# Kernel optimization log

Hardware: AMD Instinct MI355X
Metric: run time of the kernel (lower is better)

The kernel has to match this reference:

```python
import jax, jax.numpy as jnp
import numpy as np

B, T, K, H, KS = 8, 2048, 64, 8, 5
PAD = KS - 1  # causal left padding (kernel_size - stride, stride=1)


def setup_inputs() -> dict:
    key = jax.random.key(0)
    ks = jax.random.split(key, 6)
    s = 0.02
    return {
        "x": jax.random.normal(ks[0], (B, T, K), jnp.float32),
        "wq": jax.random.normal(ks[1], (K * H, K, KS), jnp.float32) * s,
        "bq": jnp.zeros((K * H,), jnp.float32),
        "wk": jax.random.normal(ks[2], (K * H, K, KS), jnp.float32) * s,
        "bk": jnp.zeros((K * H,), jnp.float32),
        "wv": jax.random.normal(ks[3], (K * H, K, KS), jnp.float32) * s,
        "wu": jax.random.normal(ks[4], (K, K * H), jnp.float32) * s,
        "bu": jnp.zeros((K,), jnp.float32),
    }


def _causal_conv(x_bkt, w, b=None):
    # x_bkt: [b, k, t]; w: [out_ch, in_ch, ks]; left-pad for causality
    y = jax.lax.conv_general_dilated(
        x_bkt, w, window_strides=(1,), padding=[(PAD, 0)],
        dimension_numbers=("NCH", "OIH", "NCH"))
    if b is not None:
        y = y + b[None, :, None]
    return y


def reference(x, wq, bq, wk, bk, wv, wu, bu):
    b, t, k = x.shape
    xc = jnp.transpose(x, (0, 2, 1))  # [b, k, t]
    # conv output channels k*h are viewed as (k, h): head index varies fastest
    q = _causal_conv(xc, wq, bq).reshape(b, k, H, t)
    kk = _causal_conv(xc, wk, bk).reshape(b, k, H, t)
    v = _causal_conv(xc, wv).reshape(b, k, H, t)
    scale = k ** 0.25
    # scores: [b, h, t_q, t_k]
    w = jnp.einsum("bdht,bdhs->bhts", q / scale, kk / scale)
    mask = jnp.triu(jnp.ones((t, t), bool), 1)  # mask_next=True, mask_diag=False
    w = jnp.where(mask[None, None], -jnp.inf, w)
    w = jax.nn.softmax(w, axis=-1)
    out = jnp.einsum("bhts,bdhs->bthd", w, v)  # [b, t, h, k]
    out = out.reshape(b, t, H * k)  # concat order (h outer, k inner)
    return out @ wu.T + bu
```

## Files before the change

### kernel.cpp

```cpp
#include <hip/hip_runtime.h>
#include <hip/hip_bf16.h>

typedef __attribute__((ext_vector_type(8))) short bf16x8;
typedef __attribute__((ext_vector_type(4))) float f32x4;
typedef __attribute__((ext_vector_type(16))) float f32x16;
typedef __attribute__((ext_vector_type(4))) unsigned int u32x4;
typedef __attribute__((ext_vector_type(2))) unsigned int u32x2;

#define Bn 8
#define Tn 2048
#define Kn 64
#define Hn 8
#define KSn 5
#define CHn 512
#define TPADn 2052

__device__ __forceinline__ unsigned short f2bf(float f) {
    unsigned int x = __builtin_bit_cast(unsigned int, f);
    unsigned int r = (x + 0x7fffu + ((x >> 16) & 1u)) >> 16;
    return (unsigned short)r;
}

__device__ __forceinline__ unsigned int cvt_pk_bf16(float lo, float hi) {
    unsigned int r;
    asm("v_cvt_pk_bf16_f32 %0, %1, %2" : "=v"(r) : "v"(lo), "v"(hi));
    return r;
}

__device__ __forceinline__ float fast_exp2(float x) {
#if __has_builtin(__builtin_amdgcn_exp2f)
    return __builtin_amdgcn_exp2f(x);
#else
    float r;
    asm("v_exp_f32 %0, %1" : "=v"(r) : "v"(x));
    return r;
#endif
}

__device__ __forceinline__ float xhalf_max(float v) {
    return fmaxf(v, __shfl_xor(v, 32));
}
__device__ __forceinline__ float xhalf_add(float v) {
    return v + __shfl_xor(v, 32);
}

__device__ __forceinline__ u32x2 pl32swap(unsigned int x, unsigned int y) {
#if __has_builtin(__builtin_amdgcn_permlane32_swap)
    return __builtin_amdgcn_permlane32_swap(x, y, false, false);
#else
    unsigned int xs = (unsigned int)__shfl_xor((int)x, 32);
    unsigned int ys = (unsigned int)__shfl_xor((int)y, 32);
    int hi = (threadIdx.x & 63) >> 5;
    u32x2 r;
    r[0] = hi ? ys : x;
    r[1] = hi ? y : xs;
    return r;
#endif
}

__device__ __forceinline__ void gload_lds16(const void* g, void* l) {
    __builtin_amdgcn_global_load_lds(
        (const __attribute__((address_space(1))) void*)g,
        (__attribute__((address_space(3))) void*)l, 16, 0, 0);
}

__global__ void prep_kernel(const float* __restrict__ x,
                            const float* __restrict__ wq, const float* __restrict__ bq,
                            const float* __restrict__ wk, const float* __restrict__ bk,
                            const float* __restrict__ wv,
                            const float* __restrict__ wu,
                            unsigned short* __restrict__ x_pad,
                            unsigned short* __restrict__ w2q, unsigned short* __restrict__ w2k,
                            unsigned short* __restrict__ w2v,
                            unsigned short* __restrict__ wu_b,
                            float* __restrict__ bqs, float* __restrict__ bks)
{
    const float inv_scale = 0.424660900144f;
    const int N0 = Bn*TPADn*Kn;
    const int N1 = KSn*CHn*Kn;
    const int total = N0 + 3*N1 + CHn*Kn + 2*CHn;
    for (int i = blockIdx.x*blockDim.x + threadIdx.x; i < total; i += gridDim.x*blockDim.x) {
        if (i < N0) {
            int b = i / (TPADn*Kn);
            int rem = i - b*(TPADn*Kn);
            int p = rem >> 6, ic = rem & 63;
            x_pad[i] = (p < 4) ? (unsigned short)0
                               : f2bf(x[((size_t)b*Tn + (p - 4))*Kn + ic]);
            continue;
        }
        int r = i - N0;
        if (r < 3*N1) {
            int conv = r / N1; int rr = r - conv*N1;
            int j = rr / (CHn*Kn); int rc = rr - j*(CHn*Kn);
            int c = rc >> 6; int ic = rc & 63;
            const float* w = (conv==0) ? wq : ((conv==1) ? wk : wv);
            float s = (conv==2) ? 1.0f : inv_scale;
            unsigned short* dst = (conv==0) ? w2q : ((conv==1) ? w2k : w2v);
            dst[rr] = f2bf(w[(c*Kn + ic)*KSn + j] * s);
            continue;
        }
        r -= 3*N1;
        if (r < CHn*Kn) { wu_b[r] = f2bf(wu[r]); continue; }
        r -= CHn*Kn;
        if (r < CHn) { bqs[r] = bq[r]*inv_scale; continue; }
        r -= CHn;
        bks[r] = bk[r]*inv_scale;
    }
}

__global__ __launch_bounds__(256) void conv_v4(
    const unsigned short* __restrict__ x_pad,
    const unsigned short* __restrict__ w2q, const unsigned short* __restrict__ w2k,
    const unsigned short* __restrict__ w2v,
    const float* __restrict__ bqs, const float* __restrict__ bks,
    unsigned short* __restrict__ q_s, unsigned short* __restrict__ k_s,
    unsigned short* __restrict__ v_t)
{
    __shared__ __align__(16) unsigned short xs[2][72*64];
    __shared__ __align__(16) unsigned short ts[64*64];
    const int tg = blockIdx.x;
    const int c0 = blockIdx.y * 64;
    const int zz = blockIdx.z;
    const int conv = zz >> 3, b = zz & 7;
    const unsigned short* w2 = (conv==0) ? w2q : ((conv==1) ? w2k : w2v);
    const float* bias = (conv==0) ? bqs : ((conv==1) ? bks : nullptr);
    unsigned short* outp = (conv==0) ? q_s : ((conv==1) ? k_s : v_t);
    const int tid = threadIdx.x;
    const int wid = tid >> 6, l = tid & 63;
    const int lr = l & 15, lh = l >> 4;
    const int wt = wid & 1, wc = wid >> 1;

    bf16x8 wf[5][2][2];
    #pragma unroll
    for (int j = 0; j < 5; ++j)
        #pragma unroll
        for (int kk = 0; kk < 2; ++kk)
            #pragma unroll
            for (int n2 = 0; n2 < 2; ++n2)
                wf[j][kk][n2] = *(const bf16x8*)
                    &w2[(j*CHn + c0 + wc*32 + n2*16 + lr)*Kn + kk*32 + lh*8];
    float bv0 = bias ? bias[c0 + wc*32 + lr]      : 0.0f;
    float bv1 = bias ? bias[c0 + wc*32 + 16 + lr] : 0.0f;

    const int swz_row = l >> 3;
    const int src_inrow = ((l & 7) << 4) ^ (swz_row << 4);

    int buf = 0;
    {
        const char* base = (const char*)(x_pad + (size_t)b*TPADn*Kn);
        int p0 = tg*256;
        for (int i = wid; i < 9; i += 4) {
            const char* src = base + (size_t)(p0 + i*8 + swz_row)*128 + src_inrow;
            gload_lds16(src, (char*)&xs[0][0] + i*1024);
        }
    }
    __syncthreads();

    for (int tt = 0; tt < 4; ++tt) {
        const int t0 = (tg*4 + tt)*64;
        if (tt < 3) {
            const char* base = (const char*)(x_pad + (size_t)b*TPADn*Kn);
            int p0 = t0 + 64;
            for (int i = wid; i < 9; i += 4) {
                const char* src = base + (size_t)(p0 + i*8 + swz_row)*128 + src_inrow;
                gload_lds16(src, (char*)&xs[buf^1][0] + i*1024);
            }
        }
        const char* xb = (const char*)&xs[buf][0];
        f32x4 acc[2][2] = {};
        #pragma unroll
        for (int j = 0; j < 5; ++j)
            #pragma unroll
            for (int kk = 0; kk < 2; ++kk) {
                #pragma unroll
                for (int m = 0; m < 2; ++m) {
                    int row = wt*32 + m*16 + lr + j;
                    bf16x8 a = *(const bf16x8*)
                        (xb + row*128 + ((kk*64 + lh*16) ^ ((row & 7) << 4)));
                    acc[m][0] = __builtin_amdgcn_mfma_f32_16x16x32_bf16(a, wf[j][kk][0], acc[m][0], 0, 0, 0);
                    acc[m][1] = __builtin_amdgcn_mfma_f32_16x16x32_bf16(a, wf[j][kk][1], acc[m][1], 0, 0, 0);
                }
            }
        __syncthreads();
        #pragma unroll
        for (int m = 0; m < 2; ++m)
            #pragma unroll
            for (int n2 = 0; n2 < 2; ++n2) {
                float bv = n2 ? bv1 : bv0;
                int cl = wc*32 + n2*16 + lr;
                #pragma unroll
                for (int reg = 0; reg < 4; ++reg) {
                    int tl = wt*32 + m*16 + lh*4 + reg;
                    ts[(tl*64 + cl) ^ ((tl & 7) << 3)] = f2bf(acc[m][n2][reg] + bv);
                }
            }
        __syncthreads();
        if (conv < 2) {
            #pragma unroll
            for (int it = 0; it < 2; ++it) {
                int idx = tid + it*256;
                int tl = idx >> 3, hl = idx & 7;
                unsigned short tmp[8];
                #pragma unroll
                for (int dl = 0; dl < 8; ++dl)
                    tmp[dl] = ts[(tl*64 + hl + 8*dl) ^ ((tl & 7) << 3)];
                size_t el = ((size_t)(b*Hn + hl)*Tn + t0 + tl)*Kn + (c0 >> 3);
                *(u32x4*)&outp[el] = *(u32x4*)tmp;
            }
        } else {
            #pragma unroll
            for (int it = 0; it < 2; ++it) {
                int idx = tid + it*256;
                int tc = idx >> 6, cl2 = idx & 63;
                int hl = cl2 & 7, dl = cl2 >> 3;
                unsigned short tmp[8];
                #pragma unroll
                for (int i2 = 0; i2 < 8; ++i2)
                    tmp[i2] = ts[((tc*8 + i2)*64 + cl2) ^ (((tc*8 + i2) & 7) << 3)];
                size_t el = ((size_t)(b*Hn + hl)*Kn + (c0 >> 3) + dl)*Tn + t0 + tc*8;
                *(u32x4*)&outp[el] = *(u32x4*)tmp;
            }
        }
        buf ^= 1;
    }
}

__global__ __launch_bounds__(256, 4) void attn_kernel(
    const unsigned short* __restrict__ q_s, const unsigned short* __restrict__ k_s,
    const unsigned short* __restrict__ v_t, unsigned short* __restrict__ attn2)
{
    __shared__ __align__(16) unsigned char lds_raw[16384];
    const int tid = threadIdx.x;
    const int wid = tid >> 6, l = tid & 63;
    const int lq = l & 31, hi = l >> 5;
    const int bx = blockIdx.x;
    const int bh = (bx & 7)*8 + ((bx >> 3) & 7);
    const int s4g = (bx >> 6) & 3, g = bx >> 8;
    const int j = (g == 0) ? 15 - s4g : (g == 1) ? s4g : (g == 2) ? 8 + s4g : 7 - s4g;
    const int cmax = 4*j + 3;
    const int cw = 4*j + wid;
    const int qw = cw * 32;
    const unsigned short* qp = q_s + (size_t)bh*Tn*Kn;
    const char* kpc = (const char*)(k_s + (size_t)bh*Tn*Kn);
    const char* vpc = (const char*)(v_t + (size_t)bh*Kn*Tn);
    unsigned short* op = attn2 + (size_t)bh*Tn*Kn;
    const int qg = qw + lq;

    const int krow = wid*8 + (l >> 3);
    const char* kSrc0 = kpc + krow*128 + (((l & 7) ^ (krow & 7)) << 4);
    const char* vSrc0 = vpc + (size_t)krow*8192 + ((l >> 2) & 1)*4096
                      + ((((l & 3) ^ (krow & 3))) << 4);
    const int dstOff = wid*1024;
    auto stage = [&](int pp, int t) {
        gload_lds16(kSrc0 + (size_t)t*4096, lds_raw + pp*4096 + dstOff);
        gload_lds16(vSrc0 + (size_t)t*64,   lds_raw + 8192 + pp*4096 + dstOff);
    };

    bf16x8 qf[4];
    #pragma unroll
    for (int m = 0; m < 4; ++m)
        qf[m] = *(const bf16x8*)&qp[(qw + lq)*Kn + m*16 + hi*8];

    f32x16 o0 = (f32x16)(0.0f), o1 = (f32x16)(0.0f);
    float m_run = -1e30f, l_run = 0.f;

    const int kReadBase = lq*128;
    const int kReadSwz  = (lq & 7) << 4;
    const int vReadBase = (lq >> 1)*128 + (lq & 1)*64;
    const int vSwz = (lq >> 1) & 3;

    stage(0, 0);
    __syncthreads();
    int p = 0;
    for (int t = 0; t <= cmax; ++t) {
        if (t < cmax) stage(p ^ 1, t + 1);
        if (t <= cw) {
            const char* sK = (const char*)lds_raw + p*4096;
            const char* sV = (const char*)lds_raw + 8192 + p*4096;
            bf16x8 kbf[4], vbf[2][2];
            #pragma unroll
            for (int m = 0; m < 4; ++m)
                kbf[m] = *(const bf16x8*)(sK + kReadBase + ((m*32 + hi*16) ^ kReadSwz));
            #pragma unroll
            for (int dn = 0; dn < 2; ++dn)
                #pragma unroll
                for (int ks = 0; ks < 2; ++ks)
                    vbf[dn][ks] = *(const bf16x8*)
                        (sV + dn*2048 + vReadBase + (((ks*2 + hi) ^ vSwz) << 4));
            const int s0 = t*32;
            f32x16 s = (f32x16)(0.0f);
            __builtin_amdgcn_s_setprio(1);
            #pragma unroll
            for (int m = 0; m < 4; ++m)
                s = __builtin_amdgcn_mfma_f32_32x32x16_bf16(kbf[m], qf[m], s, 0, 0, 0);
            __builtin_amdgcn_s_setprio(0);
            if (t == cw) {
                #pragma unroll
                for (int r = 0; r < 16; ++r) {
                    int sg = s0 + (r & 3) + 8*(r >> 2) + 4*hi;
                    if (sg > qg) s[r] = -1e30f;
                }
            }
            float a8[8];
            #pragma unroll
            for (int r = 0; r < 8; ++r) a8[r] = fmaxf(s[r], s[r + 8]);
            float a4_0 = fmaxf(a8[0], a8[4]), a4_1 = fmaxf(a8[1], a8[5]);
            float a4_2 = fmaxf(a8[2], a8[6]), a4_3 = fmaxf(a8[3], a8[7]);
            float mt = fmaxf(fmaxf(a4_0, a4_1), fmaxf(a4_2, a4_3));
            mt = xhalf_max(mt);
            if (!__all(mt <= m_run + 8.0f)) {
                float mn = fmaxf(m_run, mt);
                float alpha = fast_exp2(m_run - mn);
                m_run = mn;
                l_run *= alpha;
                #pragma unroll
                for (int r = 0; r < 16; ++r) { o0[r] *= alpha; o1[r] *= alpha; }
            }
            float ps[4] = {0.f, 0.f, 0.f, 0.f};
            #pragma unroll
            for (int r = 0; r < 16; ++r) {
                float pv = fast_exp2(s[r] - m_run);
                s[r] = pv;
                ps[r & 3] += pv;
            }
            l_run += (ps[0] + ps[1]) + (ps[2] + ps[3]);
            unsigned int W[8];
            #pragma unroll
            for (int rp = 0; rp < 8; ++rp)
                W[rp] = cvt_pk_bf16(s[2*rp], s[2*rp + 1]);
            u32x4 bw[2];
            #pragma unroll
            for (int m = 0; m < 2; ++m)
                #pragma unroll
                for (int jp = 0; jp < 2; ++jp) {
                    u32x2 sw = pl32swap(W[jp + 4*m], W[jp + 4*m + 2]);
                    bw[m][jp]     = sw[0];
                    bw[m][jp + 2] = sw[1];
                }
            __builtin_amdgcn_s_setprio(1);
            o0 = __builtin_amdgcn_mfma_f32_32x32x16_bf16(vbf[0][0], __builtin_bit_cast(bf16x8, bw[0]), o0, 0, 0, 0);
            o0 = __builtin_amdgcn_mfma_f32_32x32x16_bf16(vbf[0][1], __builtin_bit_cast(bf16x8, bw[1]), o0, 0, 0, 0);
            o1 = __builtin_amdgcn_mfma_f32_32x32x16_bf16(vbf[1][0], __builtin_bit_cast(bf16x8, bw[0]), o1, 0, 0, 0);
            o1 = __builtin_amdgcn_mfma_f32_32x32x16_bf16(vbf[1][1], __builtin_bit_cast(bf16x8, bw[1]), o1, 0, 0, 0);
            __builtin_amdgcn_s_setprio(0);
        }
        __syncthreads();
        p ^= 1;
    }

    float l_full = xhalf_add(l_run);
    char* myLds = (char*)lds_raw + wid*4096;
    float inv_l = 1.0f / l_full;
    #pragma unroll
    for (int e = 0; e < 16; e += 2) {
        int dd = (e & 3) + 8*(e >> 2) + 4*hi;
        unsigned int wv0 = cvt_pk_bf16(o0[e]*inv_l, o0[e+1]*inv_l);
        *(unsigned int*)(myLds + ((lq*128 + dd*2)      ^ ((lq & 7) << 4))) = wv0;
        unsigned int wv1 = cvt_pk_bf16(o1[e]*inv_l, o1[e+1]*inv_l);
        *(unsigned int*)(myLds + ((lq*128 + 64 + dd*2) ^ ((lq & 7) << 4))) = wv1;
    }
    int q2 = l >> 1, hf = l & 1;
    #pragma unroll
    for (int o4 = 0; o4 < 4; ++o4) {
        u32x4 vr2 = *(u32x4*)(myLds + ((q2*128 + hf*64 + o4*16) ^ ((q2 & 7) << 4)));
        *(u32x4*)&op[(qw + q2)*Kn + hf*32 + o4*8] = vr2;
    }
}

__global__ __launch_bounds__(256) void proj_kernel(
    const unsigned short* __restrict__ attn, const unsigned short* __restrict__ wu_b,
    const float* __restrict__ bu, float* __restrict__ outp)
{
    __shared__ float red[4*16*66];
    const int r0 = blockIdx.x * 16;
    const int tid = threadIdx.x;
    const int w = tid >> 6, l = tid & 63;
    const int lr = l & 15, lh = l >> 4;
    f32x4 acc[4] = {};
    const int r = r0 + lr;
    const int bb = r >> 11, tt = r & 2047;
    #pragma unroll
    for (int ki = 0; ki < 4; ++ki) {
        int kk = w*4 + ki;
        int ch = kk*32 + lh*8;
        int hh = ch >> 6, dd = ch & 63;
        bf16x8 a = *(const bf16x8*)&attn[(size_t)((bb*Hn + hh)*Tn + tt)*Kn + dd];
        #pragma unroll
        for (int n = 0; n < 4; ++n) {
            bf16x8 bf = *(const bf16x8*)&wu_b[(n*16 + lr)*CHn + ch];
            acc[n] = __builtin_amdgcn_mfma_f32_16x16x32_bf16(a, bf, acc[n], 0, 0, 0);
        }
    }
    #pragma unroll
    for (int n = 0; n < 4; ++n)
        #pragma unroll
        for (int reg = 0; reg < 4; ++reg)
            red[w*1056 + (lh*4 + reg)*66 + n*16 + lr] = acc[n][reg];
    __syncthreads();
    #pragma unroll
    for (int it = 0; it < 4; ++it) {
        int idx = tid + it*256;
        int rl = idx >> 6, ko = idx & 63;
        float s = red[rl*66 + ko] + red[1056 + rl*66 + ko]
                + red[2112 + rl*66 + ko] + red[3168 + rl*66 + ko] + bu[ko];
        outp[(size_t)(r0 + rl)*Kn + ko] = s;
    }
}

extern "C" void kernel_launch(void* const* d_in, const int* in_sizes, int n_in,
                              void* d_out, int out_size, void* d_ws, size_t ws_size,
                              hipStream_t stream)
{
    const float* x  = (const float*)d_in[0];
    const float* wq = (const float*)d_in[1];
    const float* bq = (const float*)d_in[2];
    const float* wk = (const float*)d_in[3];
    const float* bk = (const float*)d_in[4];
    const float* wv = (const float*)d_in[5];
    const float* wu = (const float*)d_in[6];
    const float* bu = (const float*)d_in[7];
    float* outp = (float*)d_out;

    char* ws = (char*)d_ws;
    size_t off = 0;
    auto alloc = [&](size_t bytes) {
        char* p = ws + off;
        off = (off + bytes + 255) & ~(size_t)255;
        return p;
    };
    unsigned short* x_pad = (unsigned short*)alloc((size_t)Bn*TPADn*Kn*2);
    unsigned short* w2q  = (unsigned short*)alloc((size_t)KSn*CHn*Kn*2);
    unsigned short* w2k  = (unsigned short*)alloc((size_t)KSn*CHn*Kn*2);
    unsigned short* w2v  = (unsigned short*)alloc((size_t)KSn*CHn*Kn*2);
    unsigned short* wu_b = (unsigned short*)alloc((size_t)CHn*Kn*2);
    float*  bqs = (float*)alloc(CHn*4);
    float*  bks = (float*)alloc(CHn*4);
    unsigned short* q_s  = (unsigned short*)alloc((size_t)Bn*Hn*Tn*Kn*2);
    unsigned short* k_s  = (unsigned short*)alloc((size_t)Bn*Hn*Tn*Kn*2);
    unsigned short* v_t  = (unsigned short*)alloc((size_t)Bn*Hn*Tn*Kn*2);
    unsigned short* attn = (unsigned short*)alloc((size_t)Bn*Tn*CHn*2);

    prep_kernel<<<2048, 256, 0, stream>>>(x, wq, bq, wk, bk, wv, wu,
                                          x_pad, w2q, w2k, w2v, wu_b, bqs, bks);
    conv_v4<<<dim3(8, 8, 24), 256, 0, stream>>>(
        x_pad, w2q, w2k, w2v, bqs, bks, q_s, k_s, v_t);
    attn_kernel<<<1024, 256, 0, stream>>>(q_s, k_s, v_t, attn);
    proj_kernel<<<(Bn*Tn)/16, 256, 0, stream>>>(attn, wu_b, bu, outp);
}
```

Baseline: 113.7 us.

## Split long causal attention query blocks across KV halves with a merge kernel

Query blocks in the second half of the sequence now have their KV range split into two segments, each handled by its own workgroup. Each workgroup writes an unnormalized bf16 partial output plus its running max and sum to a scratch buffer, and a new merge kernel combines the two with a log-sum-exp rescale. The aim is to balance per-block work so the grid is no longer limited by the longest causal blocks. The cost is an extra kernel launch, scratch-buffer traffic, and bf16 rounding of the partial outputs before they are merged.

```diff
diff --git a/kernel.cpp b/kernel.cpp
--- a/kernel.cpp
+++ b/kernel.cpp
@@ -14,6 +14,7 @@
 #define KSn 5
 #define CHn 512
 #define TPADn 2052
+#define PSZ 4608
 
 __device__ __forceinline__ unsigned short f2bf(float f) {
     unsigned int x = __builtin_bit_cast(unsigned int, f);
@@ -227,18 +228,22 @@
 
 __global__ __launch_bounds__(256, 4) void attn_kernel(
     const unsigned short* __restrict__ q_s, const unsigned short* __restrict__ k_s,
-    const unsigned short* __restrict__ v_t, unsigned short* __restrict__ attn2)
+    const unsigned short* __restrict__ v_t, unsigned short* __restrict__ attn2,
+    char* __restrict__ pbuf)
 {
     __shared__ __align__(16) unsigned char lds_raw[16384];
     const int tid = threadIdx.x;
     const int wid = tid >> 6, l = tid & 63;
     const int lq = l & 31, hi = l >> 5;
     const int bx = blockIdx.x;
-    const int bh = (bx & 7)*8 + ((bx >> 3) & 7);
-    const int s4g = (bx >> 6) & 3, g = bx >> 8;
-    const int j = (g == 0) ? 15 - s4g : (g == 1) ? s4g : (g == 2) ? 8 + s4g : 7 - s4g;
-    const int cmax = 4*j + 3;
-    const int cw = 4*j + wid;
+    const int mm = bx >> 3;
+    const int bh = (bx & 7)*8 + (mm & 7);
+    const int kb = mm >> 3;
+    int q, t0, t1, seg, part;
+    if (kb < 8)       { q = 15 - kb; seg = 0; t0 = 0;  t1 = 32;      part = 1; }
+    else if (kb < 16) { q = 23 - kb; seg = 1; t0 = 32; t1 = 4*q + 4; part = 1; }
+    else              { q = 23 - kb; seg = 0; t0 = 0;  t1 = 4*q + 4; part = 0; }
+    const int cw = 4*q + wid;
     const int qw = cw * 32;
     const unsigned short* qp = q_s + (size_t)bh*Tn*Kn;
     const char* kpc = (const char*)(k_s + (size_t)bh*Tn*Kn);
@@ -269,11 +274,11 @@
     const int vReadBase = (lq >> 1)*128 + (lq & 1)*64;
     const int vSwz = (lq >> 1) & 3;
 
-    stage(0, 0);
+    stage(0, t0);
     __syncthreads();
     int p = 0;
-    for (int t = 0; t <= cmax; ++t) {
-        if (t < cmax) stage(p ^ 1, t + 1);
+    for (int t = t0; t < t1; ++t) {
+        if (t + 1 < t1) stage(p ^ 1, t + 1);
         if (t <= cw) {
             const char* sK = (const char*)lds_raw + p*4096;
             const char* sV = (const char*)lds_raw + 8192 + p*4096;
@@ -348,6 +353,22 @@
         p ^= 1;
     }
 
+    if (part) {
+        const int pidx = ((seg*64 + bh)*8 + (q - 8))*4 + wid;
+        char* pb = pbuf + (size_t)pidx*PSZ;
+        unsigned int* po32 = (unsigned int*)pb;
+        float* pml = (float*)(pb + 4096);
+        #pragma unroll
+        for (int e = 0; e < 16; e += 2) {
+            int dd = (e & 3) + 8*(e >> 2) + 4*hi;
+            po32[(dd >> 1)*32 + lq]        = cvt_pk_bf16(o0[e], o0[e+1]);
+            po32[((dd + 32) >> 1)*32 + lq] = cvt_pk_bf16(o1[e], o1[e+1]);
+        }
+        pml[l] = m_run;
+        pml[64 + l] = l_run;
+        return;
+    }
+
     float l_full = xhalf_add(l_run);
     char* myLds = (char*)lds_raw + wid*4096;
     float inv_l = 1.0f / l_full;
@@ -365,6 +386,52 @@
         u32x4 vr2 = *(u32x4*)(myLds + ((q2*128 + hf*64 + o4*16) ^ ((q2 & 7) << 4)));
         *(u32x4*)&op[(qw + q2)*Kn + hf*32 + o4*8] = vr2;
     }
+}
+
+__global__ __launch_bounds__(256) void merge_kernel(
+    const char* __restrict__ pbuf, unsigned short* __restrict__ attn2)
+{
+    const int bx = blockIdx.x;
+    const int bh = (bx & 7)*8 + ((bx >> 3) & 7);
+    const int qq = (bx >> 6) & 7;
+    const int tid = threadIdx.x;
+    const int wid = tid >> 6, l = tid & 63;
+    const int c = 4*(8 + qq) + wid;
+    const int qw = c*32;
+    const int lq2 = l >> 1, hd = l & 1;
+
+    const int p0i = ((0*64 + bh)*8 + qq)*4 + wid;
+    const int p1i = ((1*64 + bh)*8 + qq)*4 + wid;
+    const char* pb0 = pbuf + (size_t)p0i*PSZ;
+    const char* pb1 = pbuf + (size_t)p1i*PSZ;
+    const unsigned int* po0 = (const unsigned int*)pb0;
+    const unsigned int* po1 = (const unsigned int*)pb1;
+    const float* pml0 = (const float*)(pb0 + 4096);
+    const float* pml1 = (const float*)(pb1 + 4096);
+
+    float m0 = pml0[lq2], l0 = pml0[64 + lq2] + pml0[96 + lq2];
+    float m1 = pml1[lq2], l1 = pml1[64 + lq2] + pml1[96 + lq2];
+    float mf = fmaxf(m0, m1);
+    float w0 = fast_exp2(m0 - mf), w1 = fast_exp2(m1 - mf);
+    float inv_l = 1.0f / (w0*l0 + w1*l1);
+    w0 *= inv_l; w1 *= inv_l;
+
+    unsigned int outw[16];
+    #pragma unroll
+    for (int dpl = 0; dpl < 16; ++dpl) {
+        int dp = hd*16 + dpl;
+        unsigned int v0 = po0[dp*32 + lq2];
+        unsigned int v1 = po1[dp*32 + lq2];
+        float a_lo = __builtin_bit_cast(float, v0 << 16);
+        float a_hi = __builtin_bit_cast(float, v0 & 0xffff0000u);
+        float b_lo = __builtin_bit_cast(float, v1 << 16);
+        float b_hi = __builtin_bit_cast(float, v1 & 0xffff0000u);
+        outw[dpl] = cvt_pk_bf16(w0*a_lo + w1*b_lo, w0*a_hi + w1*b_hi);
+    }
+    unsigned short* orow = attn2 + (size_t)bh*Tn*Kn + (size_t)(qw + lq2)*Kn + hd*32;
+    #pragma unroll
+    for (int o4 = 0; o4 < 4; ++o4)
+        *(u32x4*)&orow[o4*8] = *(const u32x4*)&outw[o4*4];
 }
 
 __global__ __launch_bounds__(256) void proj_kernel(
@@ -439,11 +506,13 @@
     unsigned short* k_s  = (unsigned short*)alloc((size_t)Bn*Hn*Tn*Kn*2);
     unsigned short* v_t  = (unsigned short*)alloc((size_t)Bn*Hn*Tn*Kn*2);
     unsigned short* attn = (unsigned short*)alloc((size_t)Bn*Tn*CHn*2);
+    char* pbuf = alloc((size_t)2*64*8*4*PSZ);
 
     prep_kernel<<<2048, 256, 0, stream>>>(x, wq, bq, wk, bk, wv, wu,
                                           x_pad, w2q, w2k, w2v, wu_b, bqs, bks);
     conv_v4<<<dim3(8, 8, 24), 256, 0, stream>>>(
         x_pad, w2q, w2k, w2v, bqs, bks, q_s, k_s, v_t);
-    attn_kernel<<<1024, 256, 0, stream>>>(q_s, k_s, v_t, attn);
+    attn_kernel<<<1536, 256, 0, stream>>>(q_s, k_s, v_t, attn, pbuf);
+    merge_kernel<<<512, 256, 0, stream>>>(pbuf, attn);
     proj_kernel<<<(Bn*Tn)/16, 256, 0, stream>>>(attn, wu_b, bu, outp);
 }
```

After: 120.4 us. +5.9%, slower.
